# Optimization experiments

Measured on AMD Instinct MI355X. Metric: run time of the kernel, lower is better.

The kernel has to match this reference:

```python
import jax, jax.numpy as jnp
import numpy as np

B, H, T, IN, OUT = 128, 512, 1024, 8, 2


def _likelihood(tm, arms):
    # tm: (B,), arms: (B,2) -> squared normalized timing mismatch, zeroed where tm==0
    pr = jnp.square((tm[:, None] - arms) / (0.15 * arms))
    return jnp.where(tm[:, None] == 0, jnp.zeros_like(pr), pr)


def setup_inputs() -> dict:
    key = jax.random.key(0)
    k_in, k_wi, k_wr, k_wk = jax.random.split(key, 4)
    # arms/timing strictly positive in [0.5, 1.5) to avoid division blow-up
    inputs = jax.random.uniform(k_in, (B, IN, T), dtype=jnp.float32) + 0.5
    W_in = jax.random.normal(k_wi, (H, IN), dtype=jnp.float32) / np.sqrt(IN)
    b_in = jnp.zeros((H,), jnp.float32)
    W_rec = jax.random.normal(k_wr, (H, H), dtype=jnp.float32) / np.sqrt(H)
    b_rec = jnp.zeros((H,), jnp.float32)
    W_key = jax.random.normal(k_wk, (OUT, H), dtype=jnp.float32) / np.sqrt(H)
    b_key = jnp.zeros((OUT,), jnp.float32)
    return {"inputs": inputs, "W_in": W_in, "b_in": b_in, "W_rec": W_rec,
            "b_rec": b_rec, "W_key": W_key, "b_key": b_key}


def reference(inputs, W_in, b_in, W_rec, b_rec, W_key, b_key):
    Bs, _, Ts = inputs.shape
    Hs = W_rec.shape[0]
    xs = jnp.transpose(inputs[:, :, 1:], (2, 0, 1))  # (T-1, B, 8), loop starts at t=1
    h0 = jnp.zeros((Bs, Hs), inputs.dtype)
    key0 = jnp.ones((Bs,), inputs.dtype)  # key_h_pre initialized to ones

    def step(carry, x):
        h_pre, key_pre = carry
        arms_pri = x[:, :2]
        arms_sec = x[:, 2:6]
        tm = x[:, 6:8]
        # gate secondary arms by previous key value
        arms_sum = arms_sec[:, :2] * key_pre[:, None] + arms_sec[:, 2:] * (1.0 - key_pre[:, None])
        pr = jnp.concatenate([_likelihood(tm[:, 0], arms_pri),
                              _likelihood(tm[:, 1], arms_sum)], axis=1)  # (B,4)
        h = jnp.tanh(x @ W_in.T + b_in + h_pre @ W_rec.T + b_rec)  # (B,H)
        key = jax.nn.sigmoid(h @ W_key.T + b_key)  # (B,2)
        return (h, key[:, 0]), (key, pr, h)

    _, (keys_s, prs_s, hs_s) = jax.lax.scan(step, (h0, key0), xs)

    def to_out(y):
        # (T-1, B, C) -> (B, C, T) with zeros at t=0 (buffers were torch.zeros)
        y = jnp.transpose(y, (1, 2, 0))
        return jnp.concatenate([jnp.zeros(y.shape[:2] + (1,), y.dtype), y], axis=2)

    keys = to_out(keys_s)   # (B, 2, T)
    prs = to_out(prs_s)     # (B, 4, T)
    hs = to_out(hs_s)       # (B, H, T)
    return keys, prs, hs
```

## Files before the change

kernel.cpp:

```cpp
#include <hip/hip_runtime.h>
#include <math.h>


#define BB  128
#define HH  512
#define TT  1024
#define SS  1023
#define NIN 8
#define NG  64
#define BPG 2
#define NJB 4
#define JBS 128
#define NTH 512
#define HBH (NG * BPG * HH)

#define BAR_LGKM() do {                                          \
    __builtin_amdgcn_sched_barrier(0);                           \
    __asm__ volatile("s_waitcnt lgkmcnt(0)" ::: "memory");       \
    __builtin_amdgcn_s_barrier();                                \
    __builtin_amdgcn_sched_barrier(0);                           \
} while (0)

__device__ __forceinline__ float bcast(float v, int ln) {
    return __int_as_float(__builtin_amdgcn_readlane(__float_as_int(v), ln));
}

__launch_bounds__(NTH, 2)
__global__ void rnn_persist(const float* __restrict__ inputs,
                            const float* __restrict__ W_in,
                            const float* __restrict__ b_in,
                            const float* __restrict__ W_rec,
                            const float* __restrict__ b_rec,
                            const float* __restrict__ W_key,
                            const float* __restrict__ b_key,
                            float* __restrict__ out,
                            float* __restrict__ hbuf)
{
    const int tid  = threadIdx.x;
    const int lane = tid & 63;
    const int wv   = tid >> 6;
    const int g    = blockIdx.x & (NG - 1);
    const int jb   = blockIdx.x >> 6;
    const int b0   = g * BPG;
    const int j0   = jb * JBS;

    float* keys_out = out;
    float* prs_out  = out + (size_t)BB * 2 * TT;
    float* hs_out   = out + (size_t)BB * 6 * TT;

    __shared__ float lds_chunk[8][BPG][64];
    __shared__ float lds_part[8][BPG][JBS];
    __shared__ float lds_hs[BPG * JBS * 33];
    __shared__ float lds_win[NIN][JBS];
    __shared__ float lds_wkey[2 * HH];
    __shared__ float lds_bias[JBS];
    __shared__ float lds_x2[2][BPG][NIN];
    __shared__ float lds_key[BPG];
    __shared__ float lds_bkey[2];

    float4 w0[16], w1[16];
    {
        const float4* wr0 = (const float4*)(W_rec + (size_t)(j0 + lane) * HH + wv * 64);
        const float4* wr1 = (const float4*)(W_rec + (size_t)(j0 + 64 + lane) * HH + wv * 64);
        #pragma unroll
        for (int i = 0; i < 16; ++i) { w0[i] = wr0[i]; w1[i] = wr1[i]; }
    }
    for (int r = tid; r < NIN * JBS; r += NTH) {
        int i = r & 7, j = r >> 3;
        lds_win[i][j] = W_in[(size_t)(j0 + j) * NIN + i];
    }
    for (int i = tid; i < 2 * HH; i += NTH) lds_wkey[i] = W_key[i];
    if (tid < JBS) lds_bias[tid] = b_in[j0 + tid] + b_rec[j0 + tid];
    if (tid < BPG) lds_key[tid] = 1.0f;
    if (tid < 2)   lds_bkey[tid] = b_key[tid];
    for (int r = tid; r < BPG * JBS; r += NTH) lds_hs[r * 33] = 0.0f;

    if (jb == 0) {
        if (tid < BPG * 2) keys_out[((size_t)(b0 + (tid >> 1)) * 2 + (tid & 1)) * TT] = 0.0f;
        if (tid < BPG * 4) prs_out [((size_t)(b0 + (tid >> 2)) * 4 + (tid & 3)) * TT] = 0.0f;
    }

    const float* psrc = hbuf + (size_t)g * (BPG * HH) + wv * 64 + lane;
    float*       pdst = hbuf + (size_t)g * (BPG * HH);

    __syncthreads();

    for (int s = 0; s < SS; ++s) {
        if (tid >= NTH - 16) {
            int t = tid - (NTH - 16), b = t >> 3, i = t & 7;
            lds_x2[s & 1][b][i] = inputs[(size_t)(b0 + b) * NIN * TT + (size_t)i * TT + (s + 1)];
        }
        float h0, h1;
        if (s > 0) {
            const float* p = psrc + (size_t)((s - 1) & 1) * HBH;
            const int neg = ((s - 1) >> 1) & 1;
            const float off = neg ? -3.0f : 3.0f;
            float v0, v1;
            int rdy;
            do {
                v0 = __hip_atomic_load(p,      __ATOMIC_RELAXED, __HIP_MEMORY_SCOPE_AGENT);
                v1 = __hip_atomic_load(p + HH, __ATOMIC_RELAXED, __HIP_MEMORY_SCOPE_AGENT);
                rdy = neg ? ((v0 <= -1.5f) & (v1 <= -1.5f))
                          : ((v0 >=  1.5f) & (v1 >=  1.5f));
            } while (!__all(rdy));
            h0 = v0 - off;
            h1 = v1 - off;
        } else {
            h0 = 0.0f;
            h1 = 0.0f;
        }
        if (jb == 0) {
            lds_chunk[wv][0][lane] = h0;
            lds_chunk[wv][1][lane] = h1;
        }

        {
            float a00 = 0.f, a01 = 0.f, a10 = 0.f, a11 = 0.f;
            #pragma unroll
            for (int q = 0; q < 16; ++q) {
                const float* wa = (const float*)&w0[q];
                const float* wb = (const float*)&w1[q];
                #pragma unroll
                for (int c = 0; c < 4; ++c) {
                    const int ln = q * 4 + c;
                    float s0 = bcast(h0, ln);
                    float s1 = bcast(h1, ln);
                    float wva = wa[c];
                    float wvb = wb[c];
                    a00 += wva * s0; a01 += wva * s1;
                    a10 += wvb * s0; a11 += wvb * s1;
                }
            }
            lds_part[wv][0][lane]      = a00;
            lds_part[wv][1][lane]      = a01;
            lds_part[wv][0][lane + 64] = a10;
            lds_part[wv][1][lane + 64] = a11;
        }
        BAR_LGKM();

        if (tid < BPG * JBS) {
            int b = tid >> 7, j = tid & 127;
            float pre = lds_bias[j];
            #pragma unroll
            for (int w = 0; w < 8; ++w) pre += lds_part[w][b][j];
            #pragma unroll
            for (int i = 0; i < NIN; ++i) pre += lds_x2[s & 1][b][i] * lds_win[i][j];
            float hv = tanhf(pre);
            float enc = hv + (((s >> 1) & 1) ? -3.0f : 3.0f);
            __hip_atomic_store(&pdst[(size_t)(s & 1) * HBH + (size_t)b * HH + j0 + j], enc,
                               __ATOMIC_RELAXED, __HIP_MEMORY_SCOPE_AGENT);
            lds_hs[(b * JBS + j) * 33 + ((s + 1) & 31)] = hv;
        } else if (jb == 0 && s > 0 && tid < 384) {
            int t2  = tid - 256;
            int dot = t2 >> 5;
            int b = dot >> 1, c = dot & 1, seg = t2 & 31;
            float p = 0.f;
            #pragma unroll
            for (int m = 0; m < 16; ++m) {
                int k = seg + 32 * m;
                p += lds_chunk[k >> 6][b][k & 63] * lds_wkey[c * HH + k];
            }
            #pragma unroll
            for (int off = 16; off > 0; off >>= 1) p += __shfl_down(p, off, 32);
            if (seg == 0) {
                float kv = 1.0f / (1.0f + __expf(-(p + lds_bkey[c])));
                keys_out[((size_t)(b0 + b) * 2 + c) * TT + s] = kv;
                if (c == 0) lds_key[b] = kv;
            }
        }
        BAR_LGKM();

        if (jb == 0 && tid < BPG * 4) {
            int b = tid >> 2, c = tid & 3;
            float kv = lds_key[b];
            const float* xb = lds_x2[s & 1][b];
            float tmv, arm;
            if (c < 2) { tmv = xb[6]; arm = xb[c]; }
            else       { tmv = xb[7]; arm = xb[c] * kv + xb[c + 2] * (1.0f - kv); }
            float r = (tmv - arm) / (0.15f * arm);
            prs_out[((size_t)(b0 + b) * 4 + c) * TT + (s + 1)] = (tmv == 0.0f) ? 0.0f : r * r;
        }

        if (((s + 1) & 31) == 31) {
            int u0 = s - 30;
            int r = tid >> 1, half = tid & 1;
            int b = r >> 7, j = r & 127;
            float* dst = hs_out + ((size_t)(b0 + b) * HH + j0 + j) * TT + u0 + half * 16;
            const float* src = &lds_hs[r * 33 + half * 16];
            #pragma unroll
            for (int q = 0; q < 4; ++q) {
                float4 v = { src[4 * q], src[4 * q + 1], src[4 * q + 2], src[4 * q + 3] };
                *(float4*)(dst + 4 * q) = v;
            }
        }
    }

    if (jb == 0 && tid >= 256 && tid < 384) {
        int t2  = tid - 256;
        int dot = t2 >> 5;
        int b = dot >> 1, c = dot & 1, seg = t2 & 31;
        const float* hb = hbuf + (size_t)((SS - 1) & 1) * HBH
                        + (size_t)g * (BPG * HH) + (size_t)b * HH;
        float p = 0.f;
        #pragma unroll
        for (int m = 0; m < 16; ++m) {
            int k = seg + 32 * m;
            float v;
            do {
                v = __hip_atomic_load(hb + k, __ATOMIC_RELAXED, __HIP_MEMORY_SCOPE_AGENT);
            } while (!(v <= -1.5f));
            p += (v + 3.0f) * lds_wkey[c * HH + k];
        }
        #pragma unroll
        for (int off = 16; off > 0; off >>= 1) p += __shfl_down(p, off, 32);
        if (seg == 0) {
            float kv = 1.0f / (1.0f + __expf(-(p + lds_bkey[c])));
            keys_out[((size_t)(b0 + b) * 2 + c) * TT + (TT - 1)] = kv;
        }
    }
}

extern "C" void kernel_launch(void* const* d_in, const int* in_sizes, int n_in,
                              void* d_out, int out_size, void* d_ws, size_t ws_size,
                              hipStream_t stream) {
    const float* inputs = (const float*)d_in[0];
    const float* W_in   = (const float*)d_in[1];
    const float* b_in   = (const float*)d_in[2];
    const float* W_rec  = (const float*)d_in[3];
    const float* b_rec  = (const float*)d_in[4];
    const float* W_key  = (const float*)d_in[5];
    const float* b_key  = (const float*)d_in[6];
    float* outp = (float*)d_out;

    float* hbuf = (float*)d_ws;
    hipMemsetAsync(d_ws, 0, (size_t)2 * HBH * sizeof(float), stream);

    rnn_persist<<<dim3(NG * NJB), dim3(NTH), 0, stream>>>(
        inputs, W_in, b_in, W_rec, b_rec, W_key, b_key, outp, hbuf);
}
```

Baseline: 2.571 ms.

## Restructure recurrent matvec to row-per-wave-slice with LDS-broadcast hidden state

```diff
diff --git a/kernel.cpp b/kernel.cpp
--- a/kernel.cpp
+++ b/kernel.cpp
@@ -13,6 +13,7 @@
 #define JBS 128
 #define NTH 512
 #define HBH (NG * BPG * HH)
+#define KQP 132
 
 #define BAR_LGKM() do {                                          \
     __builtin_amdgcn_sched_barrier(0);                           \
@@ -43,56 +44,58 @@
     const int jb   = blockIdx.x >> 6;
     const int b0   = g * BPG;
     const int j0   = jb * JBS;
+    const int r    = lane & 15;
+    const int kq   = lane >> 4;
+    const int lrow = wv * 16 + r;
 
     float* keys_out = out;
     float* prs_out  = out + (size_t)BB * 2 * TT;
     float* hs_out   = out + (size_t)BB * 6 * TT;
 
-    __shared__ float lds_chunk[8][BPG][64];
-    __shared__ float lds_part[8][BPG][JBS];
+    __shared__ float lds_h[2][BPG][4 * KQP];
     __shared__ float lds_hs[BPG * JBS * 33];
     __shared__ float lds_win[NIN][JBS];
     __shared__ float lds_wkey[2 * HH];
     __shared__ float lds_bias[JBS];
     __shared__ float lds_x2[2][BPG][NIN];
-    __shared__ float lds_key[BPG];
     __shared__ float lds_bkey[2];
 
-    float4 w0[16], w1[16];
+    float4 wq[32];
     {
-        const float4* wr0 = (const float4*)(W_rec + (size_t)(j0 + lane) * HH + wv * 64);
-        const float4* wr1 = (const float4*)(W_rec + (size_t)(j0 + 64 + lane) * HH + wv * 64);
+        const float4* wr = (const float4*)(W_rec + (size_t)(j0 + lrow) * HH + kq * 128);
         #pragma unroll
-        for (int i = 0; i < 16; ++i) { w0[i] = wr0[i]; w1[i] = wr1[i]; }
-    }
-    for (int r = tid; r < NIN * JBS; r += NTH) {
-        int i = r & 7, j = r >> 3;
+        for (int i = 0; i < 32; ++i) wq[i] = wr[i];
+    }
+    for (int q = tid; q < NIN * JBS; q += NTH) {
+        int i = q & 7, j = q >> 3;
         lds_win[i][j] = W_in[(size_t)(j0 + j) * NIN + i];
     }
     for (int i = tid; i < 2 * HH; i += NTH) lds_wkey[i] = W_key[i];
     if (tid < JBS) lds_bias[tid] = b_in[j0 + tid] + b_rec[j0 + tid];
-    if (tid < BPG) lds_key[tid] = 1.0f;
     if (tid < 2)   lds_bkey[tid] = b_key[tid];
-    for (int r = tid; r < BPG * JBS; r += NTH) lds_hs[r * 33] = 0.0f;
+    for (int q = tid; q < BPG * JBS; q += NTH) lds_hs[q * 33] = 0.0f;
 
     if (jb == 0) {
         if (tid < BPG * 2) keys_out[((size_t)(b0 + (tid >> 1)) * 2 + (tid & 1)) * TT] = 0.0f;
         if (tid < BPG * 4) prs_out [((size_t)(b0 + (tid >> 2)) * 4 + (tid & 3)) * TT] = 0.0f;
     }
 
-    const float* psrc = hbuf + (size_t)g * (BPG * HH) + wv * 64 + lane;
+    const int   kpoll = wv * 64 + lane;
+    const int   sq    = kpoll >> 7;
+    const int   sj    = kpoll & 127;
+    const float* psrc = hbuf + (size_t)g * (BPG * HH) + kpoll;
     float*       pdst = hbuf + (size_t)g * (BPG * HH);
 
     __syncthreads();
 
     for (int s = 0; s < SS; ++s) {
+        const int bufp = (s + 1) & 1;
         if (tid >= NTH - 16) {
             int t = tid - (NTH - 16), b = t >> 3, i = t & 7;
             lds_x2[s & 1][b][i] = inputs[(size_t)(b0 + b) * NIN * TT + (size_t)i * TT + (s + 1)];
         }
-        float h0, h1;
         if (s > 0) {
-            const float* p = psrc + (size_t)((s - 1) & 1) * HBH;
+            const float* p = psrc + (size_t)bufp * HBH;
             const int neg = ((s - 1) >> 1) & 1;
             const float off = neg ? -3.0f : 3.0f;
             float v0, v1;
@@ -103,90 +106,89 @@
                 rdy = neg ? ((v0 <= -1.5f) & (v1 <= -1.5f))
                           : ((v0 >=  1.5f) & (v1 >=  1.5f));
             } while (!__all(rdy));
-            h0 = v0 - off;
-            h1 = v1 - off;
+            lds_h[bufp][0][sq * KQP + sj] = v0 - off;
+            lds_h[bufp][1][sq * KQP + sj] = v1 - off;
         } else {
-            h0 = 0.0f;
-            h1 = 0.0f;
-        }
-        if (jb == 0) {
-            lds_chunk[wv][0][lane] = h0;
-            lds_chunk[wv][1][lane] = h1;
-        }
-
+            lds_h[bufp][0][sq * KQP + sj] = 0.0f;
+            lds_h[bufp][1][sq * KQP + sj] = 0.0f;
+        }
+        BAR_LGKM();
+
+        float a0 = 0.f, a1 = 0.f;
         {
-            float a00 = 0.f, a01 = 0.f, a10 = 0.f, a11 = 0.f;
+            const float4* h40 = (const float4*)&lds_h[bufp][0][kq * KQP];
+            const float4* h41 = (const float4*)&lds_h[bufp][1][kq * KQP];
             #pragma unroll
-            for (int q = 0; q < 16; ++q) {
-                const float* wa = (const float*)&w0[q];
-                const float* wb = (const float*)&w1[q];
+            for (int q = 0; q < 32; ++q) {
+                float4 w = wq[q];
+                float4 x0 = h40[q], x1 = h41[q];
+                a0 += w.x * x0.x + w.y * x0.y + w.z * x0.z + w.w * x0.w;
+                a1 += w.x * x1.x + w.y * x1.y + w.z * x1.z + w.w * x1.w;
+            }
+        }
+        a0 += __shfl_xor(a0, 16); a1 += __shfl_xor(a1, 16);
+        a0 += __shfl_xor(a0, 32); a1 += __shfl_xor(a1, 32);
+
+        if (lane < 16) {
+            float pre0 = a0 + lds_bias[lrow];
+            float pre1 = a1 + lds_bias[lrow];
+            #pragma unroll
+            for (int i = 0; i < NIN; ++i) {
+                float wi = lds_win[i][lrow];
+                pre0 += lds_x2[s & 1][0][i] * wi;
+                pre1 += lds_x2[s & 1][1][i] * wi;
+            }
+            float h0 = tanhf(pre0), h1 = tanhf(pre1);
+            float tagoff = ((s >> 1) & 1) ? -3.0f : 3.0f;
+            __hip_atomic_store(&pdst[(size_t)(s & 1) * HBH + j0 + lrow], h0 + tagoff,
+                               __ATOMIC_RELAXED, __HIP_MEMORY_SCOPE_AGENT);
+            __hip_atomic_store(&pdst[(size_t)(s & 1) * HBH + HH + j0 + lrow], h1 + tagoff,
+                               __ATOMIC_RELAXED, __HIP_MEMORY_SCOPE_AGENT);
+            int slot = (s + 1) & 31;
+            lds_hs[lrow * 33 + slot]               = h0;
+            lds_hs[(JBS + lrow) * 33 + slot]       = h1;
+        }
+
+        if (jb == 0 && wv == 7) {
+            float kv = 1.0f;
+            int quad = lane >> 4, kb = quad >> 1, kc = quad & 1, seg = lane & 15;
+            if (s > 0) {
+                float p = 0.f;
                 #pragma unroll
-                for (int c = 0; c < 4; ++c) {
-                    const int ln = q * 4 + c;
-                    float s0 = bcast(h0, ln);
-                    float s1 = bcast(h1, ln);
-                    float wva = wa[c];
-                    float wvb = wb[c];
-                    a00 += wva * s0; a01 += wva * s1;
-                    a10 += wvb * s0; a11 += wvb * s1;
+                for (int m = 0; m < 32; ++m) {
+                    int k = seg + 16 * m;
+                    p += lds_h[bufp][kb][(k >> 7) * KQP + (k & 127)] * lds_wkey[kc * HH + k];
                 }
-            }
-            lds_part[wv][0][lane]      = a00;
-            lds_part[wv][1][lane]      = a01;
-            lds_part[wv][0][lane + 64] = a10;
-            lds_part[wv][1][lane + 64] = a11;
-        }
-        BAR_LGKM();
-
-        if (tid < BPG * JBS) {
-            int b = tid >> 7, j = tid & 127;
-            float pre = lds_bias[j];
-            #pragma unroll
-            for (int w = 0; w < 8; ++w) pre += lds_part[w][b][j];
-            #pragma unroll
-            for (int i = 0; i < NIN; ++i) pre += lds_x2[s & 1][b][i] * lds_win[i][j];
-            float hv = tanhf(pre);
-            float enc = hv + (((s >> 1) & 1) ? -3.0f : 3.0f);
-            __hip_atomic_store(&pdst[(size_t)(s & 1) * HBH + (size_t)b * HH + j0 + j], enc,
-                               __ATOMIC_RELAXED, __HIP_MEMORY_SCOPE_AGENT);
-            lds_hs[(b * JBS + j) * 33 + ((s + 1) & 31)] = hv;
-        } else if (jb == 0 && s > 0 && tid < 384) {
-            int t2  = tid - 256;
-            int dot = t2 >> 5;
-            int b = dot >> 1, c = dot & 1, seg = t2 & 31;
-            float p = 0.f;
-            #pragma unroll
-            for (int m = 0; m < 16; ++m) {
-                int k = seg + 32 * m;
-                p += lds_chunk[k >> 6][b][k & 63] * lds_wkey[c * HH + k];
-            }
-            #pragma unroll
-            for (int off = 16; off > 0; off >>= 1) p += __shfl_down(p, off, 32);
-            if (seg == 0) {
-                float kv = 1.0f / (1.0f + __expf(-(p + lds_bkey[c])));
-                keys_out[((size_t)(b0 + b) * 2 + c) * TT + s] = kv;
-                if (c == 0) lds_key[b] = kv;
-            }
-        }
-        BAR_LGKM();
-
-        if (jb == 0 && tid < BPG * 4) {
-            int b = tid >> 2, c = tid & 3;
-            float kv = lds_key[b];
-            const float* xb = lds_x2[s & 1][b];
-            float tmv, arm;
-            if (c < 2) { tmv = xb[6]; arm = xb[c]; }
-            else       { tmv = xb[7]; arm = xb[c] * kv + xb[c + 2] * (1.0f - kv); }
-            float r = (tmv - arm) / (0.15f * arm);
-            prs_out[((size_t)(b0 + b) * 4 + c) * TT + (s + 1)] = (tmv == 0.0f) ? 0.0f : r * r;
+                p += __shfl_xor(p, 1); p += __shfl_xor(p, 2);
+                p += __shfl_xor(p, 4); p += __shfl_xor(p, 8);
+                kv = 1.0f / (1.0f + __expf(-(p + lds_bkey[kc])));
+                if (seg == 0)
+                    keys_out[((size_t)(b0 + kb) * 2 + kc) * TT + s] = kv;
+            }
+            float k0 = bcast(kv, 0);
+            float k1 = bcast(kv, 32);
+            if (lane < BPG * 4) {
+                int b = lane >> 2, c = lane & 3;
+                float kvb = b ? k1 : k0;
+                const float* xb = lds_x2[s & 1][b];
+                float tmv, arm;
+                if (c < 2) { tmv = xb[6]; arm = xb[c]; }
+                else       { tmv = xb[7]; arm = xb[c] * kvb + xb[c + 2] * (1.0f - kvb); }
+                float rr = (tmv - arm) / (0.15f * arm);
+                prs_out[((size_t)(b0 + b) * 4 + c) * TT + (s + 1)] = (tmv == 0.0f) ? 0.0f : rr * rr;
+            }
         }
 
         if (((s + 1) & 31) == 31) {
+            __builtin_amdgcn_sched_barrier(0);
+            __asm__ volatile("s_waitcnt lgkmcnt(0)" ::: "memory");
             int u0 = s - 30;
-            int r = tid >> 1, half = tid & 1;
-            int b = r >> 7, j = r & 127;
-            float* dst = hs_out + ((size_t)(b0 + b) * HH + j0 + j) * TT + u0 + half * 16;
-            const float* src = &lds_hs[r * 33 + half * 16];
+            int rb = lane >> 1, half = lane & 1;
+            int b = rb >> 4, rr2 = rb & 15;
+            int row_l = b * JBS + wv * 16 + rr2;
+            float* dst = hs_out + ((size_t)(b0 + b) * HH + j0 + wv * 16 + rr2) * TT
+                       + u0 + half * 16;
+            const float* src = &lds_hs[row_l * 33 + half * 16];
             #pragma unroll
             for (int q = 0; q < 4; ++q) {
                 float4 v = { src[4 * q], src[4 * q + 1], src[4 * q + 2], src[4 * q + 3] };
@@ -195,27 +197,25 @@
         }
     }
 
-    if (jb == 0 && tid >= 256 && tid < 384) {
-        int t2  = tid - 256;
-        int dot = t2 >> 5;
-        int b = dot >> 1, c = dot & 1, seg = t2 & 31;
+    if (jb == 0 && wv == 7) {
+        int quad = lane >> 4, kb = quad >> 1, kc = quad & 1, seg = lane & 15;
         const float* hb = hbuf + (size_t)((SS - 1) & 1) * HBH
-                        + (size_t)g * (BPG * HH) + (size_t)b * HH;
+                        + (size_t)g * (BPG * HH) + (size_t)kb * HH;
         float p = 0.f;
         #pragma unroll
-        for (int m = 0; m < 16; ++m) {
-            int k = seg + 32 * m;
+        for (int m = 0; m < 32; ++m) {
+            int k = seg + 16 * m;
             float v;
             do {
                 v = __hip_atomic_load(hb + k, __ATOMIC_RELAXED, __HIP_MEMORY_SCOPE_AGENT);
             } while (!(v <= -1.5f));
-            p += (v + 3.0f) * lds_wkey[c * HH + k];
-        }
-        #pragma unroll
-        for (int off = 16; off > 0; off >>= 1) p += __shfl_down(p, off, 32);
+            p += (v + 3.0f) * lds_wkey[kc * HH + k];
+        }
+        p += __shfl_xor(p, 1); p += __shfl_xor(p, 2);
+        p += __shfl_xor(p, 4); p += __shfl_xor(p, 8);
         if (seg == 0) {
-            float kv = 1.0f / (1.0f + __expf(-(p + lds_bkey[c])));
-            keys_out[((size_t)(b0 + b) * 2 + c) * TT + (TT - 1)] = kv;
+            float kv = 1.0f / (1.0f + __expf(-(p + lds_bkey[kc])));
+            keys_out[((size_t)(b0 + kb) * 2 + kc) * TT + (TT - 1)] = kv;
         }
     }
 }
```

New measurement: 3.538 ms. 1.38x slower.
